# Performance work log

Measured on AMD Instinct MI355X. Metric: run time of the kernel, lower is better.

## Reference

```python
import jax, jax.numpy as jnp
import numpy as np

EMBED_DIM = 2048
N_HEADS = 16
HEAD_DIM = EMBED_DIM // N_HEADS


def setup_inputs() -> dict:
    key = jax.random.key(0)
    ks = jax.random.split(key, 5)
    s = 1.0 / np.sqrt(EMBED_DIM)
    x = jax.random.normal(ks[0], (2, 2048, EMBED_DIM), dtype=jnp.float32)
    W_qkv = jax.random.uniform(ks[1], (EMBED_DIM, 3 * EMBED_DIM), jnp.float32, -s, s)
    b_qkv = jax.random.uniform(ks[2], (3 * EMBED_DIM,), jnp.float32, -s, s)
    W_out = jax.random.uniform(ks[3], (EMBED_DIM, EMBED_DIM), jnp.float32, -s, s)
    b_out = jax.random.uniform(ks[4], (EMBED_DIM,), jnp.float32, -s, s)
    return {"x": x, "W_qkv": W_qkv, "b_qkv": b_qkv, "W_out": W_out, "b_out": b_out}


def reference(x, W_qkv, b_qkv, W_out, b_out):
    batch, seq_len, _ = x.shape
    qkv = jnp.einsum('bsd,de->bse', x, W_qkv) + b_qkv
    q, k, v = jnp.split(qkv, 3, axis=-1)
    # [b, h, s, hd]
    def heads(t):
        return t.reshape(batch, seq_len, N_HEADS, HEAD_DIM).transpose(0, 2, 1, 3)
    q, k, v = heads(q), heads(k), heads(v)
    scale = 1.0 / np.sqrt(HEAD_DIM)
    scores = jnp.einsum('bhqd,bhkd->bhqk', q, k) * scale  # [b,h,s,s]
    causal = jnp.tril(jnp.ones((seq_len, seq_len), dtype=bool))
    scores = jnp.where(causal, scores, -jnp.inf)
    attn = jax.nn.softmax(scores, axis=-1)
    out = jnp.einsum('bhqk,bhkd->bhqd', attn, v)
    out = out.transpose(0, 2, 1, 3).reshape(batch, seq_len, EMBED_DIM)
    return jnp.einsum('bsd,de->bse', out, W_out) + b_out
```

## Files before the change

kernel.cpp:

```cpp
#include <hip/hip_runtime.h>
#include <hip/hip_bf16.h>

#define EMBED  2048
#define SEQ    2048
#define BATCH  2
#define NHEADS 16
#define HDIM   128
#define QKVC   (3*EMBED)
#define ROWS   (BATCH*SEQ)

typedef __attribute__((ext_vector_type(8))) short bf16x8;
typedef __attribute__((ext_vector_type(4))) float f32x4;
typedef __attribute__((ext_vector_type(16))) float f32x16;

typedef const __attribute__((address_space(1))) void* gptr1_t;
typedef __attribute__((address_space(3))) void* lptr3_t;

__device__ __forceinline__ void gld16(const unsigned short* g, unsigned short* l) {
  __builtin_amdgcn_global_load_lds((gptr1_t)g, (lptr3_t)l, 16, 0, 0);
}

__device__ __forceinline__ unsigned short f2bf(float f) {
  unsigned int x = __float_as_uint(f);
  unsigned int r = (x + 0x7fffu + ((x >> 16) & 1u)) >> 16;
  return (unsigned short)r;
}

__global__ void cast_kernel(const float* __restrict__ in, unsigned short* __restrict__ out, int n4) {
  int i = blockIdx.x * 256 + threadIdx.x;
  if (i >= n4) return;
  float4 v = reinterpret_cast<const float4*>(in)[i];
  ushort4 o;
  o.x = f2bf(v.x); o.y = f2bf(v.y); o.z = f2bf(v.z); o.w = f2bf(v.w);
  reinterpret_cast<ushort4*>(out)[i] = o;
}

__global__ void transpose_cast_kernel(const float* __restrict__ in, unsigned short* __restrict__ out,
                                      int R, int C) {
  __shared__ float tile[32][33];
  int tx = threadIdx.x & 31, ty = threadIdx.x >> 5;
  int c0 = blockIdx.x * 32, r0 = blockIdx.y * 32;
  #pragma unroll
  for (int i = 0; i < 32; i += 8)
    tile[ty + i][tx] = in[(size_t)(r0 + ty + i) * C + c0 + tx];
  __syncthreads();
  #pragma unroll
  for (int i = 0; i < 32; i += 8)
    out[(size_t)(c0 + ty + i) * R + r0 + tx] = f2bf(tile[tx][ty + i]);
}

template<int MODE>
__global__ __launch_bounds__(256)
void gemm_kernel(const unsigned short* __restrict__ A,
                 const unsigned short* __restrict__ BT,
                 const float* __restrict__ bias,
                 unsigned short* __restrict__ outb,
                 unsigned short* __restrict__ vt,
                 float* __restrict__ outf,
                 int M, int N, int K) {
  __shared__ unsigned short As[2 * 128 * 32];
  __shared__ unsigned short Bs[2 * 128 * 32];
  const int t = threadIdx.x;
  const int lane = t & 63, wave = t >> 6;
  const int l31 = lane & 31, hl = lane >> 5;
  const int wm = wave >> 1, wn = wave & 1;
  const int m0 = blockIdx.y * 128, n0 = blockIdx.x * 128;

  f32x16 acc[2][2] = {};

  int aoff[2][4], boff[2][4];
  #pragma unroll
  for (int i = 0; i < 2; ++i) {
    int m = wm * 64 + i * 32 + l31;
    int pm = ((m >> 2) ^ m) & 3;
    int n = wn * 64 + i * 32 + l31;
    int pn = ((n >> 2) ^ n) & 3;
    #pragma unroll
    for (int s4 = 0; s4 < 4; ++s4) {
      int st = s4 >> 1, c = (s4 & 1) * 2 + hl;
      aoff[i][s4] = st * 4096 + (m * 4 + (c ^ pm)) * 8;
      boff[i][s4] = st * 4096 + (n * 4 + (c ^ pn)) * 8;
    }
  }
  int ldso[4];
  const unsigned short* Ag[4];
  const unsigned short* Bg[4];
  #pragma unroll
  for (int i = 0; i < 4; ++i) {
    int cc = i * 256 + t;
    int st = cc >> 9, w = cc & 511;
    int r = w >> 2, s = w & 3;
    int d = s ^ (((r >> 2) ^ r) & 3);
    ldso[i] = st * 4096 + w * 8;
    Ag[i] = A  + (size_t)(m0 + r) * K + st * 32 + d * 8;
    Bg[i] = BT + (size_t)(n0 + r) * K + st * 32 + d * 8;
  }

  for (int k0 = 0; k0 < K; k0 += 64) {
    #pragma unroll
    for (int i = 0; i < 4; ++i) gld16(Ag[i] + k0, &As[ldso[i]]);
    #pragma unroll
    for (int i = 0; i < 4; ++i) gld16(Bg[i] + k0, &Bs[ldso[i]]);
    __syncthreads();
    #pragma unroll
    for (int s4 = 0; s4 < 4; ++s4) {
      bf16x8 a0 = *(const bf16x8*)&As[aoff[0][s4]];
      bf16x8 a1 = *(const bf16x8*)&As[aoff[1][s4]];
      bf16x8 b0 = *(const bf16x8*)&Bs[boff[0][s4]];
      bf16x8 b1 = *(const bf16x8*)&Bs[boff[1][s4]];
      acc[0][0] = __builtin_amdgcn_mfma_f32_32x32x16_bf16(a0, b0, acc[0][0], 0, 0, 0);
      acc[0][1] = __builtin_amdgcn_mfma_f32_32x32x16_bf16(a0, b1, acc[0][1], 0, 0, 0);
      acc[1][0] = __builtin_amdgcn_mfma_f32_32x32x16_bf16(a1, b0, acc[1][0], 0, 0, 0);
      acc[1][1] = __builtin_amdgcn_mfma_f32_32x32x16_bf16(a1, b1, acc[1][1], 0, 0, 0);
    }
    __syncthreads();
  }

  #pragma unroll
  for (int i = 0; i < 2; ++i) {
    int rowb = m0 + wm * 64 + i * 32 + 4 * hl;
    #pragma unroll
    for (int j = 0; j < 2; ++j) {
      int col = n0 + wn * 64 + j * 32 + l31;
      float bv = bias[col];
      if (MODE == 1) {
        #pragma unroll
        for (int g = 0; g < 4; ++g)
          #pragma unroll
          for (int rr = 0; rr < 4; ++rr)
            outf[(size_t)(rowb + 8 * g + rr) * N + col] = acc[i][j][4 * g + rr] + bv;
      } else if (n0 < 2 * EMBED) {
        #pragma unroll
        for (int g = 0; g < 4; ++g)
          #pragma unroll
          for (int rr = 0; rr < 4; ++rr)
            outb[(size_t)(rowb + 8 * g + rr) * 4096 + col] = f2bf(acc[i][j][4 * g + rr] + bv);
      } else {
        int hd = col - 2 * EMBED;
        int b = rowb >> 11;
        int sbase = rowb & 2047;
        #pragma unroll
        for (int g = 0; g < 4; ++g) {
          ushort4 w;
          w.x = f2bf(acc[i][j][4 * g + 0] + bv);
          w.y = f2bf(acc[i][j][4 * g + 1] + bv);
          w.z = f2bf(acc[i][j][4 * g + 2] + bv);
          w.w = f2bf(acc[i][j][4 * g + 3] + bv);
          *(ushort4*)&vt[(((size_t)(b << 11) + hd) << 11) + sbase + 8 * g] = w;
        }
      }
    }
  }
}

__global__ __launch_bounds__(256)
void attn_kernel(const unsigned short* __restrict__ qk,
                 const unsigned short* __restrict__ vt,
                 unsigned short* __restrict__ outb) {
  __shared__ unsigned short Ks[2][64 * 128];
  __shared__ unsigned short Vs[2][64 * 128];
  __shared__ unsigned short Ps[4][16 * 72];
  const int t = threadIdx.x;
  const int lane = t & 63, wave = t >> 6;
  const int quad = lane >> 4, l16 = lane & 15;
  const int bh = blockIdx.x;
  const int pair = blockIdx.y;
  const int b = bh >> 4, h = bh & 15;
  const size_t rowbase = (size_t)b * SEQ;
  const int hq = h * HDIM;
  const unsigned short* vbase = vt + ((size_t)bh * HDIM) * SEQ;

  const float SC = 0.08838834764831845f * 1.4426950408889634f;

  #pragma unroll
  for (int half = 0; half < 2; ++half) {
    const int qt = half ? (31 - pair) : pair;
    const int qw0 = qt * 64 + wave * 16;

    bf16x8 qf[4];
    {
      const unsigned short* qrow = qk + (size_t)(rowbase + qw0 + l16) * 4096 + hq + quad * 8;
      #pragma unroll
      for (int s = 0; s < 4; ++s) qf[s] = *(const bf16x8*)(qrow + s * 32);
    }

    f32x4 o[8] = {};
    float mrow = -1e30f, lrow = 0.f;

    #pragma unroll
    for (int i = 0; i < 4; ++i) {
      int cc = i * 256 + t;
      int kv = cc >> 4, sc = cc & 15;
      int dc = sc ^ (kv & 15);
      gld16(qk + (size_t)(rowbase + kv) * 4096 + EMBED + hq + dc * 8, &Ks[0][cc * 8]);
    }
    #pragma unroll
    for (int i = 0; i < 4; ++i) {
      int cc = i * 256 + t;
      int d = cc >> 3, c = cc & 7;
      int dc = c ^ (d & 7);
      gld16(vbase + (size_t)d * SEQ + dc * 8, &Vs[0][cc * 8]);
    }

    for (int j = 0; j <= qt; ++j) {
      const int cur = j & 1;
      __syncthreads();

      if (j < qt) {
        const int kv1 = (j + 1) * 64;
        #pragma unroll
        for (int i = 0; i < 4; ++i) {
          int cc = i * 256 + t;
          int kv = cc >> 4, sc = cc & 15;
          int dc = sc ^ (kv & 15);
          gld16(qk + (size_t)(rowbase + kv1 + kv) * 4096 + EMBED + hq + dc * 8, &Ks[cur ^ 1][cc * 8]);
        }
        #pragma unroll
        for (int i = 0; i < 4; ++i) {
          int cc = i * 256 + t;
          int d = cc >> 3, c = cc & 7;
          int dc = c ^ (d & 7);
          gld16(vbase + (size_t)d * SEQ + kv1 + dc * 8, &Vs[cur ^ 1][cc * 8]);
        }
      }

      const int kv0 = j * 64;
      f32x4 sacc[4] = {};
      #pragma unroll
      for (int nb = 0; nb < 4; ++nb) {
        int kvr = nb * 16 + l16;
        #pragma unroll
        for (int ks = 0; ks < 4; ++ks) {
          int dc2 = (ks * 4 + quad) ^ (kvr & 15);
          bf16x8 kb = *(const bf16x8*)&Ks[cur][(kvr * 16 + dc2) * 8];
          sacc[nb] = __builtin_amdgcn_mfma_f32_16x16x32_bf16(kb, qf[ks], sacc[nb], 0, 0, 0);
        }
      }

      float p[4][4];
      float smax = -1e30f;
      if (j == qt) {
        const int qg = qw0 + l16;
        #pragma unroll
        for (int nb = 0; nb < 4; ++nb)
          #pragma unroll
          for (int r = 0; r < 4; ++r) {
            float v = sacc[nb][r] * SC;
            if ((kv0 + nb * 16 + quad * 4 + r) > qg) v = -1e30f;
            p[nb][r] = v;
            smax = fmaxf(smax, v);
          }
      } else {
        #pragma unroll
        for (int nb = 0; nb < 4; ++nb)
          #pragma unroll
          for (int r = 0; r < 4; ++r) {
            float v = sacc[nb][r] * SC;
            p[nb][r] = v;
            smax = fmaxf(smax, v);
          }
      }
      smax = fmaxf(smax, __shfl_xor(smax, 16));
      smax = fmaxf(smax, __shfl_xor(smax, 32));

      const float mold = mrow;
      const unsigned long long grew = __ballot(smax > mold);
      const float mnew = fmaxf(mold, smax);
      mrow = mnew;

      float rs = 0.f;
      #pragma unroll
      for (int nb = 0; nb < 4; ++nb)
        #pragma unroll
        for (int r = 0; r < 4; ++r) {
          float pv = exp2f(p[nb][r] - mnew);
          p[nb][r] = pv;
          rs += pv;
        }
      rs += __shfl_xor(rs, 16);
      rs += __shfl_xor(rs, 32);

      unsigned short* pw = &Ps[wave][0];
      #pragma unroll
      for (int nb = 0; nb < 4; ++nb) {
        __hip_bfloat162 lo = __float22bfloat162_rn(make_float2(p[nb][0], p[nb][1]));
        __hip_bfloat162 hi = __float22bfloat162_rn(make_float2(p[nb][2], p[nb][3]));
        ushort4 w;
        w.x = *(unsigned short*)&lo.x; w.y = *(unsigned short*)&lo.y;
        w.z = *(unsigned short*)&hi.x; w.w = *(unsigned short*)&hi.y;
        *(ushort4*)&pw[l16 * 72 + nb * 16 + quad * 4] = w;
      }

      if (grew) {
        float alpha = exp2f(mold - mnew);
        lrow = lrow * alpha + rs;
        #pragma unroll
        for (int r = 0; r < 4; ++r) {
          float av = __shfl(alpha, quad * 4 + r, 16);
          #pragma unroll
          for (int db = 0; db < 8; ++db) o[db][r] *= av;
        }
      } else {
        lrow += rs;
      }

      asm volatile("s_waitcnt lgkmcnt(0)" ::: "memory");
      bf16x8 pa[2];
      #pragma unroll
      for (int ks2 = 0; ks2 < 2; ++ks2)
        pa[ks2] = *(const bf16x8*)&pw[l16 * 72 + ks2 * 32 + quad * 8];

      #pragma unroll
      for (int db = 0; db < 8; ++db) {
        int d = db * 16 + l16;
        #pragma unroll
        for (int ks2 = 0; ks2 < 2; ++ks2) {
          int dc = (ks2 * 4 + quad) ^ (d & 7);
          bf16x8 vb = *(const bf16x8*)&Vs[cur][(d * 8 + dc) * 8];
          o[db] = __builtin_amdgcn_mfma_f32_16x16x32_bf16(pa[ks2], vb, o[db], 0, 0, 0);
        }
      }
    }

    #pragma unroll
    for (int r = 0; r < 4; ++r) {
      float lr = __shfl(lrow, quad * 4 + r, 16);
      float inv = 1.0f / lr;
      size_t row = rowbase + qw0 + quad * 4 + r;
      #pragma unroll
      for (int db = 0; db < 8; ++db)
        outb[row * EMBED + hq + db * 16 + l16] = f2bf(o[db][r] * inv);
    }
    __syncthreads();
  }
}

extern "C" void kernel_launch(void* const* d_in, const int* in_sizes, int n_in,
                              void* d_out, int out_size, void* d_ws, size_t ws_size,
                              hipStream_t stream) {
  const float* x    = (const float*)d_in[0];
  const float* Wqkv = (const float*)d_in[1];
  const float* bqkv = (const float*)d_in[2];
  const float* Wout = (const float*)d_in[3];
  const float* bout = (const float*)d_in[4];
  float* out = (float*)d_out;

  unsigned short* xb    = (unsigned short*)d_ws;
  unsigned short* wqkvT = xb    + (size_t)ROWS * EMBED;
  unsigned short* woutT = wqkvT + (size_t)EMBED * QKVC;
  unsigned short* qkb   = woutT + (size_t)EMBED * EMBED;
  unsigned short* vtb   = qkb   + (size_t)ROWS * 4096;
  unsigned short* attnb = vtb   + (size_t)32 * HDIM * SEQ;

  cast_kernel<<<dim3((ROWS * EMBED / 4 + 255) / 256), 256, 0, stream>>>(x, xb, ROWS * EMBED / 4);
  transpose_cast_kernel<<<dim3(QKVC / 32, EMBED / 32), 256, 0, stream>>>(Wqkv, wqkvT, EMBED, QKVC);
  transpose_cast_kernel<<<dim3(EMBED / 32, EMBED / 32), 256, 0, stream>>>(Wout, woutT, EMBED, EMBED);

  gemm_kernel<0><<<dim3(QKVC / 128, ROWS / 128), 256, 0, stream>>>(
      xb, wqkvT, bqkv, qkb, vtb, nullptr, ROWS, QKVC, EMBED);

  attn_kernel<<<dim3(32, 16), 256, 0, stream>>>(qkb, vtb, attnb);

  gemm_kernel<1><<<dim3(EMBED / 128, ROWS / 128), 256, 0, stream>>>(
      attnb, woutT, bout, nullptr, nullptr, out, ROWS, EMBED, EMBED);
}
```

Before: 391.4 us.

## Share K/V tile loads between paired query tiles in one causal attention pass

The two query tiles a block handles (pair and 31-pair) are now processed together in a single KV loop, so each K/V tile loaded into LDS is used by both tiles instead of being reloaded in a second pass. This cuts global-to-LDS traffic and barriers for the shorter tile. In exchange each wave keeps two sets of Q fragments and output accumulators live, which raises VGPR pressure and may lower occupancy or cause spills.

```diff
diff --git a/kernel.cpp b/kernel.cpp
--- a/kernel.cpp
+++ b/kernel.cpp
@@ -172,166 +172,177 @@
 
   const float SC = 0.08838834764831845f * 1.4426950408889634f;
 
-  #pragma unroll
-  for (int half = 0; half < 2; ++half) {
-    const int qt = half ? (31 - pair) : pair;
-    const int qw0 = qt * 64 + wave * 16;
-
-    bf16x8 qf[4];
-    {
-      const unsigned short* qrow = qk + (size_t)(rowbase + qw0 + l16) * 4096 + hq + quad * 8;
-      #pragma unroll
-      for (int s = 0; s < 4; ++s) qf[s] = *(const bf16x8*)(qrow + s * 32);
-    }
-
-    f32x4 o[8] = {};
-    float mrow = -1e30f, lrow = 0.f;
-
-    #pragma unroll
-    for (int i = 0; i < 4; ++i) {
-      int cc = i * 256 + t;
-      int kv = cc >> 4, sc = cc & 15;
-      int dc = sc ^ (kv & 15);
-      gld16(qk + (size_t)(rowbase + kv) * 4096 + EMBED + hq + dc * 8, &Ks[0][cc * 8]);
-    }
-    #pragma unroll
-    for (int i = 0; i < 4; ++i) {
-      int cc = i * 256 + t;
-      int d = cc >> 3, c = cc & 7;
-      int dc = c ^ (d & 7);
-      gld16(vbase + (size_t)d * SEQ + dc * 8, &Vs[0][cc * 8]);
-    }
-
-    for (int j = 0; j <= qt; ++j) {
-      const int cur = j & 1;
-      __syncthreads();
-
-      if (j < qt) {
-        const int kv1 = (j + 1) * 64;
-        #pragma unroll
-        for (int i = 0; i < 4; ++i) {
-          int cc = i * 256 + t;
-          int kv = cc >> 4, sc = cc & 15;
-          int dc = sc ^ (kv & 15);
-          gld16(qk + (size_t)(rowbase + kv1 + kv) * 4096 + EMBED + hq + dc * 8, &Ks[cur ^ 1][cc * 8]);
+  const int qtA = pair, qtB = 31 - pair;
+  const int qw0A = qtA * 64 + wave * 16;
+  const int qw0B = qtB * 64 + wave * 16;
+
+  bf16x8 qfA[4], qfB[4];
+  {
+    const unsigned short* qrA = qk + (size_t)(rowbase + qw0A + l16) * 4096 + hq + quad * 8;
+    const unsigned short* qrB = qk + (size_t)(rowbase + qw0B + l16) * 4096 + hq + quad * 8;
+    #pragma unroll
+    for (int s = 0; s < 4; ++s) { qfA[s] = *(const bf16x8*)(qrA + s * 32); qfB[s] = *(const bf16x8*)(qrB + s * 32); }
+  }
+
+  f32x4 oA[8] = {}, oB[8] = {};
+  float mA = -1e30f, lA = 0.f, mB = -1e30f, lB = 0.f;
+
+  #pragma unroll
+  for (int i = 0; i < 4; ++i) {
+    int cc = i * 256 + t;
+    int kv = cc >> 4, sc = cc & 15;
+    int dc = sc ^ (kv & 15);
+    gld16(qk + (size_t)(rowbase + kv) * 4096 + EMBED + hq + dc * 8, &Ks[0][cc * 8]);
+  }
+  #pragma unroll
+  for (int i = 0; i < 4; ++i) {
+    int cc = i * 256 + t;
+    int d = cc >> 3, c = cc & 7;
+    int dc = c ^ (d & 7);
+    gld16(vbase + (size_t)d * SEQ + dc * 8, &Vs[0][cc * 8]);
+  }
+
+  auto process = [&](int j, int cur, int kv0, const bf16x8* qf, f32x4* o,
+                     float& mrow, float& lrow, int qt, int qw0) {
+    f32x4 sacc[4] = {};
+    #pragma unroll
+    for (int nb = 0; nb < 4; ++nb) {
+      int kvr = nb * 16 + l16;
+      #pragma unroll
+      for (int ks = 0; ks < 4; ++ks) {
+        int dc2 = (ks * 4 + quad) ^ (kvr & 15);
+        bf16x8 kb = *(const bf16x8*)&Ks[cur][(kvr * 16 + dc2) * 8];
+        sacc[nb] = __builtin_amdgcn_mfma_f32_16x16x32_bf16(kb, qf[ks], sacc[nb], 0, 0, 0);
+      }
+    }
+
+    float p[4][4];
+    float smax = -1e30f;
+    if (j == qt) {
+      const int qg = qw0 + l16;
+      #pragma unroll
+      for (int nb = 0; nb < 4; ++nb)
+        #pragma unroll
+        for (int r = 0; r < 4; ++r) {
+          float v = sacc[nb][r] * SC;
+          if ((kv0 + nb * 16 + quad * 4 + r) > qg) v = -1e30f;
+          p[nb][r] = v;
+          smax = fmaxf(smax, v);
         }
-        #pragma unroll
-        for (int i = 0; i < 4; ++i) {
-          int cc = i * 256 + t;
-          int d = cc >> 3, c = cc & 7;
-          int dc = c ^ (d & 7);
-          gld16(vbase + (size_t)d * SEQ + kv1 + dc * 8, &Vs[cur ^ 1][cc * 8]);
+    } else {
+      #pragma unroll
+      for (int nb = 0; nb < 4; ++nb)
+        #pragma unroll
+        for (int r = 0; r < 4; ++r) {
+          float v = sacc[nb][r] * SC;
+          p[nb][r] = v;
+          smax = fmaxf(smax, v);
         }
-      }
-
-      const int kv0 = j * 64;
-      f32x4 sacc[4] = {};
-      #pragma unroll
-      for (int nb = 0; nb < 4; ++nb) {
-        int kvr = nb * 16 + l16;
-        #pragma unroll
-        for (int ks = 0; ks < 4; ++ks) {
-          int dc2 = (ks * 4 + quad) ^ (kvr & 15);
-          bf16x8 kb = *(const bf16x8*)&Ks[cur][(kvr * 16 + dc2) * 8];
-          sacc[nb] = __builtin_amdgcn_mfma_f32_16x16x32_bf16(kb, qf[ks], sacc[nb], 0, 0, 0);
-        }
-      }
-
-      float p[4][4];
-      float smax = -1e30f;
-      if (j == qt) {
-        const int qg = qw0 + l16;
-        #pragma unroll
-        for (int nb = 0; nb < 4; ++nb)
-          #pragma unroll
-          for (int r = 0; r < 4; ++r) {
-            float v = sacc[nb][r] * SC;
-            if ((kv0 + nb * 16 + quad * 4 + r) > qg) v = -1e30f;
-            p[nb][r] = v;
-            smax = fmaxf(smax, v);
-          }
-      } else {
-        #pragma unroll
-        for (int nb = 0; nb < 4; ++nb)
-          #pragma unroll
-          for (int r = 0; r < 4; ++r) {
-            float v = sacc[nb][r] * SC;
-            p[nb][r] = v;
-            smax = fmaxf(smax, v);
-          }
-      }
-      smax = fmaxf(smax, __shfl_xor(smax, 16));
-      smax = fmaxf(smax, __shfl_xor(smax, 32));
-
-      const float mold = mrow;
-      const unsigned long long grew = __ballot(smax > mold);
-      const float mnew = fmaxf(mold, smax);
-      mrow = mnew;
-
-      float rs = 0.f;
-      #pragma unroll
-      for (int nb = 0; nb < 4; ++nb)
-        #pragma unroll
-        for (int r = 0; r < 4; ++r) {
-          float pv = exp2f(p[nb][r] - mnew);
-          p[nb][r] = pv;
-          rs += pv;
-        }
-      rs += __shfl_xor(rs, 16);
-      rs += __shfl_xor(rs, 32);
-
-      unsigned short* pw = &Ps[wave][0];
-      #pragma unroll
-      for (int nb = 0; nb < 4; ++nb) {
-        __hip_bfloat162 lo = __float22bfloat162_rn(make_float2(p[nb][0], p[nb][1]));
-        __hip_bfloat162 hi = __float22bfloat162_rn(make_float2(p[nb][2], p[nb][3]));
-        ushort4 w;
-        w.x = *(unsigned short*)&lo.x; w.y = *(unsigned short*)&lo.y;
-        w.z = *(unsigned short*)&hi.x; w.w = *(unsigned short*)&hi.y;
-        *(ushort4*)&pw[l16 * 72 + nb * 16 + quad * 4] = w;
-      }
-
-      if (grew) {
-        float alpha = exp2f(mold - mnew);
-        lrow = lrow * alpha + rs;
-        #pragma unroll
-        for (int r = 0; r < 4; ++r) {
-          float av = __shfl(alpha, quad * 4 + r, 16);
-          #pragma unroll
-          for (int db = 0; db < 8; ++db) o[db][r] *= av;
-        }
-      } else {
-        lrow += rs;
-      }
-
-      asm volatile("s_waitcnt lgkmcnt(0)" ::: "memory");
-      bf16x8 pa[2];
-      #pragma unroll
-      for (int ks2 = 0; ks2 < 2; ++ks2)
-        pa[ks2] = *(const bf16x8*)&pw[l16 * 72 + ks2 * 32 + quad * 8];
-
-      #pragma unroll
-      for (int db = 0; db < 8; ++db) {
-        int d = db * 16 + l16;
-        #pragma unroll
-        for (int ks2 = 0; ks2 < 2; ++ks2) {
-          int dc = (ks2 * 4 + quad) ^ (d & 7);
-          bf16x8 vb = *(const bf16x8*)&Vs[cur][(d * 8 + dc) * 8];
-          o[db] = __builtin_amdgcn_mfma_f32_16x16x32_bf16(pa[ks2], vb, o[db], 0, 0, 0);
-        }
-      }
-    }
-
-    #pragma unroll
-    for (int r = 0; r < 4; ++r) {
-      float lr = __shfl(lrow, quad * 4 + r, 16);
-      float inv = 1.0f / lr;
-      size_t row = rowbase + qw0 + quad * 4 + r;
-      #pragma unroll
-      for (int db = 0; db < 8; ++db)
-        outb[row * EMBED + hq + db * 16 + l16] = f2bf(o[db][r] * inv);
-    }
+    }
+    smax = fmaxf(smax, __shfl_xor(smax, 16));
+    smax = fmaxf(smax, __shfl_xor(smax, 32));
+
+    const float mold = mrow;
+    const unsigned long long grew = __ballot(smax > mold);
+    const float mnew = fmaxf(mold, smax);
+    mrow = mnew;
+
+    float rs = 0.f;
+    #pragma unroll
+    for (int nb = 0; nb < 4; ++nb)
+      #pragma unroll
+      for (int r = 0; r < 4; ++r) {
+        float pv = exp2f(p[nb][r] - mnew);
+        p[nb][r] = pv;
+        rs += pv;
+      }
+    rs += __shfl_xor(rs, 16);
+    rs += __shfl_xor(rs, 32);
+
+    unsigned short* pw = &Ps[wave][0];
+    #pragma unroll
+    for (int nb = 0; nb < 4; ++nb) {
+      __hip_bfloat162 lo = __float22bfloat162_rn(make_float2(p[nb][0], p[nb][1]));
+      __hip_bfloat162 hi = __float22bfloat162_rn(make_float2(p[nb][2], p[nb][3]));
+      ushort4 w;
+      w.x = *(unsigned short*)&lo.x; w.y = *(unsigned short*)&lo.y;
+      w.z = *(unsigned short*)&hi.x; w.w = *(unsigned short*)&hi.y;
+      *(ushort4*)&pw[l16 * 72 + nb * 16 + quad * 4] = w;
+    }
+
+    if (grew) {
+      float alpha = exp2f(mold - mnew);
+      lrow = lrow * alpha + rs;
+      #pragma unroll
+      for (int r = 0; r < 4; ++r) {
+        float av = __shfl(alpha, quad * 4 + r, 16);
+        #pragma unroll
+        for (int db = 0; db < 8; ++db) o[db][r] *= av;
+      }
+    } else {
+      lrow += rs;
+    }
+
+    asm volatile("s_waitcnt lgkmcnt(0)" ::: "memory");
+    bf16x8 pa[2];
+    #pragma unroll
+    for (int ks2 = 0; ks2 < 2; ++ks2)
+      pa[ks2] = *(const bf16x8*)&pw[l16 * 72 + ks2 * 32 + quad * 8];
+
+    #pragma unroll
+    for (int db = 0; db < 8; ++db) {
+      int d = db * 16 + l16;
+      #pragma unroll
+      for (int ks2 = 0; ks2 < 2; ++ks2) {
+        int dc = (ks2 * 4 + quad) ^ (d & 7);
+        bf16x8 vb = *(const bf16x8*)&Vs[cur][(d * 8 + dc) * 8];
+        o[db] = __builtin_amdgcn_mfma_f32_16x16x32_bf16(pa[ks2], vb, o[db], 0, 0, 0);
+      }
+    }
+  };
+
+  for (int j = 0; j <= qtB; ++j) {
+    const int cur = j & 1;
     __syncthreads();
+
+    if (j < qtB) {
+      const int kv1 = (j + 1) * 64;
+      #pragma unroll
+      for (int i = 0; i < 4; ++i) {
+        int cc = i * 256 + t;
+        int kv = cc >> 4, sc = cc & 15;
+        int dc = sc ^ (kv & 15);
+        gld16(qk + (size_t)(rowbase + kv1 + kv) * 4096 + EMBED + hq + dc * 8, &Ks[cur ^ 1][cc * 8]);
+      }
+      #pragma unroll
+      for (int i = 0; i < 4; ++i) {
+        int cc = i * 256 + t;
+        int d = cc >> 3, c = cc & 7;
+        int dc = c ^ (d & 7);
+        gld16(vbase + (size_t)d * SEQ + kv1 + dc * 8, &Vs[cur ^ 1][cc * 8]);
+      }
+    }
+
+    const int kv0 = j * 64;
+    process(j, cur, kv0, qfB, oB, mB, lB, qtB, qw0B);
+    if (j <= qtA)
+      process(j, cur, kv0, qfA, oA, mA, lA, qtA, qw0A);
+  }
+
+  #pragma unroll
+  for (int r = 0; r < 4; ++r) {
+    float lrB = __shfl(lB, quad * 4 + r, 16);
+    float invB = 1.0f / lrB;
+    size_t rowB = rowbase + qw0B + quad * 4 + r;
+    #pragma unroll
+    for (int db = 0; db < 8; ++db)
+      outb[rowB * EMBED + hq + db * 16 + l16] = f2bf(oB[db][r] * invB);
+    float lrA = __shfl(lA, quad * 4 + r, 16);
+    float invA = 1.0f / lrA;
+    size_t rowA = rowbase + qw0A + quad * 4 + r;
+    #pragma unroll
+    for (int db = 0; db < 8; ++db)
+      outb[rowA * EMBED + hq + db * 16 + l16] = f2bf(oA[db][r] * invA);
   }
 }
 
```

Measured after the change: 414.1 us. 1.06x slower.
